# Optimization experiments

Measured on AMD Instinct MI355X. Metric: run time of the kernel, lower is better.

The kernel has to match this reference:

```python
import jax, jax.numpy as jnp
import numpy as np

D_MODEL = 512
D_STATE = 32
EXPAND = 2
D_INNER = D_MODEL * EXPAND
BATCH = 2
SEQ_LEN = 1024


def setup_inputs() -> dict:
    key = jax.random.key(0)
    ks = jax.random.split(key, 8)
    s = lambda fan_in: 1.0 / np.sqrt(fan_in)
    x = jax.random.normal(ks[0], (BATCH, SEQ_LEN, D_MODEL), dtype=jnp.float32)
    Wx = jax.random.uniform(ks[1], (D_INNER, D_MODEL), minval=-s(D_MODEL), maxval=s(D_MODEL))
    Wdt = jax.random.uniform(ks[2], (D_INNER, D_MODEL), minval=-s(D_MODEL), maxval=s(D_MODEL))
    bdt = jax.random.uniform(ks[3], (D_INNER,)) + 1.0  # dt_proj.bias init: rand + 1
    A_log = jnp.log(jax.random.uniform(ks[4], (D_INNER, D_STATE), minval=1e-4, maxval=1.0))
    WB = jax.random.uniform(ks[5], (D_INNER * D_STATE, D_MODEL), minval=-s(D_MODEL), maxval=s(D_MODEL))
    WC = jax.random.uniform(ks[6], (D_INNER * D_STATE, D_MODEL), minval=-s(D_MODEL), maxval=s(D_MODEL))
    Wout = jax.random.uniform(ks[7], (D_MODEL, D_INNER), minval=-s(D_INNER), maxval=s(D_INNER))
    return {"x": x, "Wx": Wx, "Wdt": Wdt, "bdt": bdt, "A_log": A_log,
            "WB": WB, "WC": WC, "Wout": Wout}


def reference(x, Wx, Wdt, bdt, A_log, WB, WC, Wout):
    b, L, _ = x.shape
    d_inner, d_state = A_log.shape

    x_inner = jnp.einsum('bld,ed->ble', x, Wx)                 # (b, L, d_inner)
    delta = jax.nn.softplus(jnp.einsum('bld,ed->ble', x, Wdt) + bdt)
    A = -jnp.exp(A_log.astype(jnp.float32))                    # (d_inner, d_state)
    A_disc = jnp.exp(delta[..., None] * A)                     # (b, L, d_inner, d_state)
    Bm = jnp.einsum('bld,ed->ble', x, WB).reshape(b, L, d_inner, d_state)
    Cm = jnp.einsum('bld,ed->ble', x, WC).reshape(b, L, d_inner, d_state)

    def step(h, inp):
        a_t, b_t, c_t, x_t = inp
        h = a_t * h + b_t * x_t[..., None]                     # (b, d_inner, d_state)
        y = jnp.sum(c_t * h, axis=-1)                          # (b, d_inner)
        return h, y

    h0 = jnp.zeros((b, d_inner, d_state), dtype=x.dtype)
    xs = (jnp.moveaxis(A_disc, 1, 0), jnp.moveaxis(Bm, 1, 0),
          jnp.moveaxis(Cm, 1, 0), jnp.moveaxis(x_inner, 1, 0))
    _, ys = jax.lax.scan(step, h0, xs)                         # ys: (L, b, d_inner)
    y = jnp.moveaxis(ys, 0, 1)
    y = y * jax.nn.sigmoid(y)                                  # SiLU
    return jnp.einsum('ble,de->bld', y, Wout)
```

## Files before the change

### kernel.cpp

```cpp
#include <hip/hip_runtime.h>

#define BATCH   2
#define SEQLEN  1024
#define DMODEL  512
#define DSTATE  32
#define DINNER  1024
#define MROWS   (BATCH*SEQLEN)
#define NPROJ   (2*DINNER + 2*DINNER*DSTATE)

typedef short bf16x8 __attribute__((ext_vector_type(8)));
typedef float f32x4  __attribute__((ext_vector_type(4)));

__device__ __forceinline__ unsigned short f2bf(float f) {
    union { float f; unsigned u; } c; c.f = f;
    unsigned u = c.u;
    u += 0x7fffu + ((u >> 16) & 1u);
    return (unsigned short)(u >> 16);
}
__device__ __forceinline__ float bf2f(unsigned short h) {
    union { unsigned u; float f; } c; c.u = ((unsigned)h) << 16;
    return c.f;
}

__global__ void cast_all(const float4* __restrict__ Wx, const float4* __restrict__ Wdt,
                         const float4* __restrict__ WB, const float4* __restrict__ WC,
                         const float4* __restrict__ x,  const float4* __restrict__ Wout,
                         unsigned short* __restrict__ Wbf,
                         unsigned short* __restrict__ Xbf,
                         unsigned short* __restrict__ Woutbf) {
    const long nWx = 131072, nWdt = 131072, nWB = 4194304, nWC = 4194304;
    const long nWall = nWx + nWdt + nWB + nWC;
    const long nX = 262144, nWo = 131072;
    const long total = nWall + nX + nWo;
    for (long u = (long)blockIdx.x * blockDim.x + threadIdx.x; u < total;
         u += (long)gridDim.x * blockDim.x) {
        float4 v; unsigned short* dst;
        if (u < nWall) {
            if (u < nWx)             v = Wx[u];
            else if (u < nWx+nWdt)   v = Wdt[u - nWx];
            else if (u < nWx+nWdt+nWB) v = WB[u - nWx - nWdt];
            else                     v = WC[u - nWx - nWdt - nWB];
            dst = Wbf + u*4;
        } else if (u < nWall + nX) {
            v = x[u - nWall];       dst = Xbf + (u - nWall)*4;
        } else {
            v = Wout[u - nWall - nX]; dst = Woutbf + (u - nWall - nX)*4;
        }
        ushort4 o; o.x = f2bf(v.x); o.y = f2bf(v.y); o.z = f2bf(v.z); o.w = f2bf(v.w);
        *(ushort4*)dst = o;
    }
}

template<int EPI>
__global__ __launch_bounds__(256)
void gemm_bt(const unsigned short* __restrict__ A, const unsigned short* __restrict__ Bw,
             int K, int N, int t0, int Tchunk, int tgs,
             float* __restrict__ xin, float* __restrict__ dlt,
             unsigned short* __restrict__ Bout, unsigned short* __restrict__ Cout,
             const float* __restrict__ bdt, float* __restrict__ outf) {
    __shared__ unsigned short Asm[2][128*32];
    __shared__ unsigned short Bsm[2][128*32];
    const int tid  = threadIdx.x;
    const int w    = tid >> 6;
    const int lane = tid & 63;
    const int wm   = w >> 1, wn = w & 1;

    const int nx = gridDim.x, ny = gridDim.y;
    int ntile, rtile;
    if ((nx & 7) == 0) {
        const int lin = blockIdx.x + nx * blockIdx.y;
        const int xcd = lin & 7;
        const int sl  = lin >> 3;
        ntile = xcd * (nx >> 3) + sl / ny;
        rtile = sl % ny;
    } else {
        ntile = blockIdx.x; rtile = blockIdx.y;
    }

    const int rr0  = rtile * 128;
    const int bb   = (rr0 >= Tchunk) ? 1 : 0;
    const int grow0 = bb * SEQLEN + t0 + (rr0 - bb * Tchunk);
    const int n0   = ntile * 128;

    f32x4 acc[4][4] = {};

    const unsigned short* Ag = A  + (size_t)grow0 * K;
    const unsigned short* Bg = Bw + (size_t)n0 * K;

    const int c0 = w*64 + lane;
    const int c1 = c0 + 256;
    const int r   = lane & 15;
    const int h16 = lane >> 4;

    const int rowc0 = c0 >> 2, rowc1 = c1 >> 2;
    const int subc0 = (c0 & 3) ^ ((c0 >> 3) & 3);
    const int subc1 = (c1 & 3) ^ ((c1 >> 3) & 3);
    const size_t srcA0 = (size_t)rowc0 * K + subc0 * 8;
    const size_t srcA1 = (size_t)rowc1 * K + subc1 * 8;

    const int nt = K >> 5;

    #define STAGE(k0_, buf_)                                                              \
        do {                                                                              \
            __builtin_amdgcn_global_load_lds(                                             \
                (const __attribute__((address_space(1))) void*)(Ag + srcA0 + (k0_)),      \
                (__attribute__((address_space(3))) void*)(&Asm[(buf_)][w*512]), 16, 0, 0);\
            __builtin_amdgcn_global_load_lds(                                             \
                (const __attribute__((address_space(1))) void*)(Ag + srcA1 + (k0_)),      \
                (__attribute__((address_space(3))) void*)(&Asm[(buf_)][2048 + w*512]), 16, 0, 0); \
            __builtin_amdgcn_global_load_lds(                                             \
                (const __attribute__((address_space(1))) void*)(Bg + srcA0 + (k0_)),      \
                (__attribute__((address_space(3))) void*)(&Bsm[(buf_)][w*512]), 16, 0, 0);\
            __builtin_amdgcn_global_load_lds(                                             \
                (const __attribute__((address_space(1))) void*)(Bg + srcA1 + (k0_)),      \
                (__attribute__((address_space(3))) void*)(&Bsm[(buf_)][2048 + w*512]), 16, 0, 0); \
        } while (0)

    #define COMPUTE(buf_)                                                                 \
        do {                                                                              \
            bf16x8 af[4], bfr[4];                                                         \
            _Pragma("unroll")                                                             \
            for (int i = 0; i < 4; i++) {                                                 \
                const int Ra = wm*64 + i*16 + r;                                          \
                const int Rb = wn*64 + i*16 + r;                                          \
                af[i]  = *(const bf16x8*)(&Asm[(buf_)][Ra*32 + (h16 ^ ((Ra>>1)&3))*8]);   \
                bfr[i] = *(const bf16x8*)(&Bsm[(buf_)][Rb*32 + (h16 ^ ((Rb>>1)&3))*8]);   \
            }                                                                             \
            _Pragma("unroll")                                                             \
            for (int i = 0; i < 4; i++)                                                   \
                _Pragma("unroll")                                                         \
                for (int j = 0; j < 4; j++)                                               \
                    acc[i][j] = __builtin_amdgcn_mfma_f32_16x16x32_bf16(af[i], bfr[j], acc[i][j], 0, 0, 0); \
        } while (0)

    STAGE(0, 0);
    for (int it = 0; it < nt - 1; ++it) {
        const int cur = it & 1;
        STAGE((it + 1) * 32, cur ^ 1);
        asm volatile("s_waitcnt vmcnt(4)" ::: "memory");
        __builtin_amdgcn_s_barrier();
        COMPUTE(cur);
        asm volatile("" ::: "memory");
        __builtin_amdgcn_s_barrier();
        asm volatile("" ::: "memory");
    }
    asm volatile("s_waitcnt vmcnt(0)" ::: "memory");
    __builtin_amdgcn_s_barrier();
    COMPUTE((nt - 1) & 1);

    #undef STAGE
    #undef COMPUTE

    const int q = lane >> 4;
    const int Tg  = 1 << tgs;
    const int NT  = Tg >> 3;
    #pragma unroll
    for (int i = 0; i < 4; i++) {
        const int lr0 = wm*64 + i*16 + q*4;
        #pragma unroll
        for (int j = 0; j < 4; j++) {
            const int ncol = n0 + wn*64 + j*16 + r;
            if (EPI == 0) {
                const int cr   = rr0 + lr0;
                const int lt   = cr - bb*Tchunk;
                const int seg  = lt >> tgs;
                const int tloc = lt & (Tg - 1);
                const int kin  = tloc >> 3;
                const int tin  = tloc & 7;
                const int bs   = bb*8 + seg;
                if (ncol < 1024) {
                    float4 o = {acc[i][j][0], acc[i][j][1], acc[i][j][2], acc[i][j][3]};
                    *(float4*)(xin + ((size_t)bs*1024 + ncol)*Tg + tloc) = o;
                } else if (ncol < 2048) {
                    const float bias = bdt[ncol - 1024];
                    float4 o;
                    {   float z0 = acc[i][j][0] + bias; o.x = (z0 > 20.f) ? z0 : log1pf(__expf(z0));
                        float z1 = acc[i][j][1] + bias; o.y = (z1 > 20.f) ? z1 : log1pf(__expf(z1));
                        float z2 = acc[i][j][2] + bias; o.z = (z2 > 20.f) ? z2 : log1pf(__expf(z2));
                        float z3 = acc[i][j][3] + bias; o.w = (z3 > 20.f) ? z3 : log1pf(__expf(z3)); }
                    *(float4*)(dlt + ((size_t)bs*1024 + (ncol-1024))*Tg + tloc) = o;
                } else if (ncol < 34816) {
                    const int es = ncol - 2048;
                    short4 o;
                    o.x = (short)f2bf(acc[i][j][0]); o.y = (short)f2bf(acc[i][j][1]);
                    o.z = (short)f2bf(acc[i][j][2]); o.w = (short)f2bf(acc[i][j][3]);
                    *(short4*)(Bout + (((size_t)bs*1024 + (es>>5))*NT + kin)*256 + (es&31)*8 + tin) = o;
                } else {
                    const int es = ncol - 34816;
                    short4 o;
                    o.x = (short)f2bf(acc[i][j][0]); o.y = (short)f2bf(acc[i][j][1]);
                    o.z = (short)f2bf(acc[i][j][2]); o.w = (short)f2bf(acc[i][j][3]);
                    *(short4*)(Cout + (((size_t)bs*1024 + (es>>5))*NT + kin)*256 + (es&31)*8 + tin) = o;
                }
            } else {
                #pragma unroll
                for (int t = 0; t < 4; t++)
                    outf[(size_t)(grow0 + lr0 + t)*N + ncol] = acc[i][j][t];
            }
        }
    }
}

__global__ __launch_bounds__(256)
void scan_seg1(const float* __restrict__ dlt, const float* __restrict__ xin,
               const unsigned short* __restrict__ Bbf,
               const float* __restrict__ A_log,
               float* __restrict__ sc_h, float* __restrict__ sc_a,
               int Tg) {
    const int tid = threadIdx.x;
    const int g = tid >> 5, s = tid & 31;
    const int G = blockIdx.x * 8 + g;
    const int seg = blockIdx.y;
    const int b = G >> 10, e = G & 1023;

    const float Aes = -__expf(A_log[e*32 + s]);
    float h = 0.f, ap = 1.f;

    const int NT = Tg >> 3;
    const int bs = b*8 + seg;
    const float* dp = dlt + ((size_t)bs*1024 + e)*Tg;
    const float* xp = xin + ((size_t)bs*1024 + e)*Tg;
    const unsigned short* bp = Bbf + ((size_t)bs*1024 + e)*NT*256 + s*8;

    float4 d0 = *(const float4*)dp, d1 = *(const float4*)(dp+4);
    float4 x0 = *(const float4*)xp, x1 = *(const float4*)(xp+4);
    bf16x8 bv = *(const bf16x8*)bp;

    for (int k = 0; k < NT; ++k) {
        float4 nd0, nd1, nx0, nx1; bf16x8 nbv;
        if (k + 1 < NT) {
            nd0 = *(const float4*)(dp + (k+1)*8); nd1 = *(const float4*)(dp + (k+1)*8 + 4);
            nx0 = *(const float4*)(xp + (k+1)*8); nx1 = *(const float4*)(xp + (k+1)*8 + 4);
            nbv = *(const bf16x8*)(bp + (size_t)(k+1)*256);
        }
        const float db[8] = {d0.x,d0.y,d0.z,d0.w,d1.x,d1.y,d1.z,d1.w};
        const float xb[8] = {x0.x,x0.y,x0.z,x0.w,x1.x,x1.y,x1.z,x1.w};
        #pragma unroll
        for (int j = 0; j < 8; j++) {
            const float a = __expf(db[j] * Aes);
            h = a*h + bf2f((unsigned short)bv[j])*xb[j];
            ap *= a;
        }
        if (k + 1 < NT) { d0=nd0; d1=nd1; x0=nx0; x1=nx1; bv=nbv; }
    }
    sc_h[((size_t)G*8 + seg)*32 + s] = h;
    sc_a[((size_t)G*8 + seg)*32 + s] = ap;
}

__global__ __launch_bounds__(256)
void scan_seg2(const float* __restrict__ sc_h, const float* __restrict__ sc_a,
               float* __restrict__ sc_hin, float* __restrict__ hbuf,
               int first) {
    const int idx = blockIdx.x * 256 + threadIdx.x;
    float h = first ? 0.f : hbuf[idx];
    const int G = idx >> 5, s = idx & 31;
    for (int seg = 0; seg < 8; seg++) {
        const size_t o = ((size_t)G*8 + seg)*32 + s;
        sc_hin[o] = h;
        h = sc_h[o] + sc_a[o]*h;
    }
    hbuf[idx] = h;
}

__global__ __launch_bounds__(256)
void scan_seg3(const float* __restrict__ dlt, const float* __restrict__ xin,
               const unsigned short* __restrict__ Bbf, const unsigned short* __restrict__ Cbf,
               const float* __restrict__ A_log, const float* __restrict__ sc_hin,
               unsigned short* __restrict__ Ybf,
               int t0, int Tg) {
    const int tid = threadIdx.x;
    const int g = tid >> 5, s = tid & 31;
    const int G = blockIdx.x * 8 + g;
    const int seg = blockIdx.y;
    const int b = G >> 10, e = G & 1023;

    const float Aes = -__expf(A_log[e*32 + s]);
    float h = sc_hin[((size_t)G*8 + seg)*32 + s];

    const int NT = Tg >> 3;
    const int bs = b*8 + seg;
    const float* dp = dlt + ((size_t)bs*1024 + e)*Tg;
    const float* xp = xin + ((size_t)bs*1024 + e)*Tg;
    const unsigned short* bp = Bbf + ((size_t)bs*1024 + e)*NT*256 + s*8;
    const unsigned short* cp = Cbf + ((size_t)bs*1024 + e)*NT*256 + s*8;
    const int tbase = t0 + seg*Tg;

    float4 d0 = *(const float4*)dp, d1 = *(const float4*)(dp+4);
    float4 x0 = *(const float4*)xp, x1 = *(const float4*)(xp+4);
    bf16x8 bv = *(const bf16x8*)bp, cv = *(const bf16x8*)cp;

    for (int k = 0; k < NT; ++k) {
        float4 nd0, nd1, nx0, nx1; bf16x8 nbv, ncv;
        if (k + 1 < NT) {
            nd0 = *(const float4*)(dp + (k+1)*8); nd1 = *(const float4*)(dp + (k+1)*8 + 4);
            nx0 = *(const float4*)(xp + (k+1)*8); nx1 = *(const float4*)(xp + (k+1)*8 + 4);
            nbv = *(const bf16x8*)(bp + (size_t)(k+1)*256);
            ncv = *(const bf16x8*)(cp + (size_t)(k+1)*256);
        }
        const float db[8] = {d0.x,d0.y,d0.z,d0.w,d1.x,d1.y,d1.z,d1.w};
        const float xb[8] = {x0.x,x0.y,x0.z,x0.w,x1.x,x1.y,x1.z,x1.w};
        float p[8];
        #pragma unroll
        for (int j = 0; j < 8; j++) {
            const float a = __expf(db[j] * Aes);
            h = a*h + bf2f((unsigned short)bv[j])*xb[j];
            p[j] = bf2f((unsigned short)cv[j])*h;
        }
        #pragma unroll
        for (int i = 0; i < 4; i++) {
            float send = (s & 16) ? p[i] : p[i+4];
            float recv = __shfl_xor(send, 16, 32);
            p[i] = ((s & 16) ? p[i+4] : p[i]) + recv;
        }
        #pragma unroll
        for (int i = 0; i < 2; i++) {
            float send = (s & 8) ? p[i] : p[i+2];
            float recv = __shfl_xor(send, 8, 32);
            p[i] = ((s & 8) ? p[i+2] : p[i]) + recv;
        }
        {
            float send = (s & 4) ? p[0] : p[1];
            float recv = __shfl_xor(send, 4, 32);
            p[0] = ((s & 4) ? p[1] : p[0]) + recv;
        }
        p[0] += __shfl_xor(p[0], 2, 32);
        p[0] += __shfl_xor(p[0], 1, 32);
        if ((s & 3) == 0) {
            const int tl = s >> 2;
            const float qv = p[0];
            const float y = qv * __builtin_amdgcn_rcpf(1.f + __expf(-qv));
            Ybf[(size_t)b*1048576 + e + (size_t)(tbase + k*8 + tl)*1024] = f2bf(y);
        }
        if (k + 1 < NT) { d0=nd0; d1=nd1; x0=nx0; x1=nx1; bv=nbv; cv=ncv; }
    }
}

extern "C" void kernel_launch(void* const* d_in, const int* in_sizes, int n_in,
                              void* d_out, int out_size, void* d_ws, size_t ws_size,
                              hipStream_t stream) {
    const float* x     = (const float*)d_in[0];
    const float* Wx    = (const float*)d_in[1];
    const float* Wdt   = (const float*)d_in[2];
    const float* bdt   = (const float*)d_in[3];
    const float* A_log = (const float*)d_in[4];
    const float* WB    = (const float*)d_in[5];
    const float* WC    = (const float*)d_in[6];
    const float* Wout  = (const float*)d_in[7];

    char* ws = (char*)d_ws;
    unsigned short* Wbf    = (unsigned short*)(ws);
    unsigned short* Xbf    = (unsigned short*)(ws + 69206016);
    unsigned short* Woutbf = (unsigned short*)(ws + 71303168);
    float*          xin    = (float*)        (ws + 72351744);
    float*          dlt    = (float*)        (ws + 80740352);
    unsigned short* Ybf    = (unsigned short*)(ws + 89128960);
    float*          hbuf   = (float*)        (ws + 93323264);
    float*          sc_h   = (float*)        (ws + 93585408);
    float*          sc_a   = (float*)        (ws + 95682560);
    float*          sc_hin = (float*)        (ws + 97779712);
    unsigned short* Bbf    = (unsigned short*)(ws + 99876864);
    const size_t fixedB = 99876864;

    int T = 128;
    const int cands[4] = {1024, 512, 256, 128};
    for (int ci = 0; ci < 4; ci++) {
        if (fixedB + (size_t)2 * cands[ci] * 131072 <= ws_size) { T = cands[ci]; break; }
    }
    unsigned short* Cbf = Bbf + (size_t)T * 65536;

    const int Tg = T / 8;
    int tgs = 0; while ((1 << tgs) < Tg) tgs++;

    cast_all<<<dim3(2048), dim3(256), 0, stream>>>(
        (const float4*)Wx, (const float4*)Wdt, (const float4*)WB, (const float4*)WC,
        (const float4*)x, (const float4*)Wout, Wbf, Xbf, Woutbf);

    const int NC = SEQLEN / T;
    for (int c = 0; c < NC; c++) {
        const int t0 = c * T;
        gemm_bt<0><<<dim3(NPROJ/128, 2*T/128), dim3(256), 0, stream>>>(
            Xbf, Wbf, DMODEL, NPROJ, t0, T, tgs, xin, dlt, Bbf, Cbf, bdt, nullptr);
        scan_seg1<<<dim3(256, 8), dim3(256), 0, stream>>>(
            dlt, xin, Bbf, A_log, sc_h, sc_a, Tg);
        scan_seg2<<<dim3(256), dim3(256), 0, stream>>>(
            sc_h, sc_a, sc_hin, hbuf, (c == 0) ? 1 : 0);
        scan_seg3<<<dim3(256, 8), dim3(256), 0, stream>>>(
            dlt, xin, Bbf, Cbf, A_log, sc_hin, Ybf, t0, Tg);
    }

    gemm_bt<1><<<dim3(DMODEL/128, MROWS/128), dim3(256), 0, stream>>>(
        Ybf, Woutbf, DINNER, DMODEL, 0, MROWS, 0, nullptr, nullptr, nullptr, nullptr, nullptr,
        (float*)d_out);
}
```

Measured before the change: 413.8 us.

## Fuse three-pass chunked scan into one kernel with shared-memory segment carry

Replaces the three scan kernels (per-segment local scan, serial carry propagation, rescan with output) with one kernel. Each block handles one (batch, channel) row, and its 8 warps cover the 8 time segments. Segment summaries are combined through shared memory, and each warp keeps its B values in registers between the two passes so B is read from global memory once. This removes two launches per chunk and the sc_h/sc_a/sc_hin global round trips. In exchange it adds register pressure (up to 16 bf16x8 vectors per thread) and drops the explicit software prefetch of the next step's data.

```diff
diff --git a/kernel.cpp b/kernel.cpp
--- a/kernel.cpp
+++ b/kernel.cpp
@@ -201,122 +201,84 @@
     }
 }
 
+template<int NT>
 __global__ __launch_bounds__(256)
-void scan_seg1(const float* __restrict__ dlt, const float* __restrict__ xin,
-               const unsigned short* __restrict__ Bbf,
-               const float* __restrict__ A_log,
-               float* __restrict__ sc_h, float* __restrict__ sc_a,
-               int Tg) {
+void scan_fused(const float* __restrict__ dlt, const float* __restrict__ xin,
+                const unsigned short* __restrict__ Bbf, const unsigned short* __restrict__ Cbf,
+                const float* __restrict__ A_log,
+                unsigned short* __restrict__ Ybf, float* __restrict__ hbuf,
+                int t0, int first) {
     const int tid = threadIdx.x;
     const int g = tid >> 5, s = tid & 31;
-    const int G = blockIdx.x * 8 + g;
-    const int seg = blockIdx.y;
+    const int G = blockIdx.x;
     const int b = G >> 10, e = G & 1023;
+    const int bs = b*8 + g;
+    const int Tg = NT * 8;
 
     const float Aes = -__expf(A_log[e*32 + s]);
-    float h = 0.f, ap = 1.f;
-
-    const int NT = Tg >> 3;
-    const int bs = b*8 + seg;
-    const float* dp = dlt + ((size_t)bs*1024 + e)*Tg;
-    const float* xp = xin + ((size_t)bs*1024 + e)*Tg;
-    const unsigned short* bp = Bbf + ((size_t)bs*1024 + e)*NT*256 + s*8;
-
-    float4 d0 = *(const float4*)dp, d1 = *(const float4*)(dp+4);
-    float4 x0 = *(const float4*)xp, x1 = *(const float4*)(xp+4);
-    bf16x8 bv = *(const bf16x8*)bp;
-
-    for (int k = 0; k < NT; ++k) {
-        float4 nd0, nd1, nx0, nx1; bf16x8 nbv;
-        if (k + 1 < NT) {
-            nd0 = *(const float4*)(dp + (k+1)*8); nd1 = *(const float4*)(dp + (k+1)*8 + 4);
-            nx0 = *(const float4*)(xp + (k+1)*8); nx1 = *(const float4*)(xp + (k+1)*8 + 4);
-            nbv = *(const bf16x8*)(bp + (size_t)(k+1)*256);
-        }
-        const float db[8] = {d0.x,d0.y,d0.z,d0.w,d1.x,d1.y,d1.z,d1.w};
-        const float xb[8] = {x0.x,x0.y,x0.z,x0.w,x1.x,x1.y,x1.z,x1.w};
-        #pragma unroll
-        for (int j = 0; j < 8; j++) {
-            const float a = __expf(db[j] * Aes);
-            h = a*h + bf2f((unsigned short)bv[j])*xb[j];
-            ap *= a;
-        }
-        if (k + 1 < NT) { d0=nd0; d1=nd1; x0=nx0; x1=nx1; bv=nbv; }
-    }
-    sc_h[((size_t)G*8 + seg)*32 + s] = h;
-    sc_a[((size_t)G*8 + seg)*32 + s] = ap;
-}
-
-__global__ __launch_bounds__(256)
-void scan_seg2(const float* __restrict__ sc_h, const float* __restrict__ sc_a,
-               float* __restrict__ sc_hin, float* __restrict__ hbuf,
-               int first) {
-    const int idx = blockIdx.x * 256 + threadIdx.x;
-    float h = first ? 0.f : hbuf[idx];
-    const int G = idx >> 5, s = idx & 31;
-    for (int seg = 0; seg < 8; seg++) {
-        const size_t o = ((size_t)G*8 + seg)*32 + s;
-        sc_hin[o] = h;
-        h = sc_h[o] + sc_a[o]*h;
-    }
-    hbuf[idx] = h;
-}
-
-__global__ __launch_bounds__(256)
-void scan_seg3(const float* __restrict__ dlt, const float* __restrict__ xin,
-               const unsigned short* __restrict__ Bbf, const unsigned short* __restrict__ Cbf,
-               const float* __restrict__ A_log, const float* __restrict__ sc_hin,
-               unsigned short* __restrict__ Ybf,
-               int t0, int Tg) {
-    const int tid = threadIdx.x;
-    const int g = tid >> 5, s = tid & 31;
-    const int G = blockIdx.x * 8 + g;
-    const int seg = blockIdx.y;
-    const int b = G >> 10, e = G & 1023;
-
-    const float Aes = -__expf(A_log[e*32 + s]);
-    float h = sc_hin[((size_t)G*8 + seg)*32 + s];
-
-    const int NT = Tg >> 3;
-    const int bs = b*8 + seg;
+
     const float* dp = dlt + ((size_t)bs*1024 + e)*Tg;
     const float* xp = xin + ((size_t)bs*1024 + e)*Tg;
     const unsigned short* bp = Bbf + ((size_t)bs*1024 + e)*NT*256 + s*8;
     const unsigned short* cp = Cbf + ((size_t)bs*1024 + e)*NT*256 + s*8;
-    const int tbase = t0 + seg*Tg;
-
-    float4 d0 = *(const float4*)dp, d1 = *(const float4*)(dp+4);
-    float4 x0 = *(const float4*)xp, x1 = *(const float4*)(xp+4);
-    bf16x8 bv = *(const bf16x8*)bp, cv = *(const bf16x8*)cp;
-
-    for (int k = 0; k < NT; ++k) {
-        float4 nd0, nd1, nx0, nx1; bf16x8 nbv, ncv;
-        if (k + 1 < NT) {
-            nd0 = *(const float4*)(dp + (k+1)*8); nd1 = *(const float4*)(dp + (k+1)*8 + 4);
-            nx0 = *(const float4*)(xp + (k+1)*8); nx1 = *(const float4*)(xp + (k+1)*8 + 4);
-            nbv = *(const bf16x8*)(bp + (size_t)(k+1)*256);
-            ncv = *(const bf16x8*)(cp + (size_t)(k+1)*256);
-        }
+
+    bf16x8 Bc[NT];
+    #pragma unroll
+    for (int k = 0; k < NT; k++) Bc[k] = *(const bf16x8*)(bp + (size_t)k*256);
+
+    float h = 0.f, ap = 1.f;
+    #pragma unroll
+    for (int k = 0; k < NT; k++) {
+        const float4 d0 = *(const float4*)(dp + k*8), d1 = *(const float4*)(dp + k*8 + 4);
+        const float4 x0 = *(const float4*)(xp + k*8), x1 = *(const float4*)(xp + k*8 + 4);
+        const float db[8] = {d0.x,d0.y,d0.z,d0.w,d1.x,d1.y,d1.z,d1.w};
+        const float xb[8] = {x0.x,x0.y,x0.z,x0.w,x1.x,x1.y,x1.z,x1.w};
+        #pragma unroll
+        for (int j = 0; j < 8; j++) {
+            const float a = __expf(db[j] * Aes);
+            h = a*h + bf2f((unsigned short)Bc[k][j])*xb[j];
+            ap *= a;
+        }
+    }
+
+    __shared__ float Lh[8][32];
+    __shared__ float La[8][32];
+    Lh[g][s] = h; La[g][s] = ap;
+    __syncthreads();
+    float hin = first ? 0.f : hbuf[(size_t)G*32 + s];
+    #pragma unroll
+    for (int j = 0; j < 7; j++) {
+        if (j < g) hin = La[j][s]*hin + Lh[j][s];
+    }
+    if (g == 7) hbuf[(size_t)G*32 + s] = La[7][s]*hin + Lh[7][s];
+
+    h = hin;
+    const int tbase = t0 + g*Tg;
+    #pragma unroll
+    for (int k = 0; k < NT; k++) {
+        const bf16x8 cv = *(const bf16x8*)(cp + (size_t)k*256);
+        const float4 d0 = *(const float4*)(dp + k*8), d1 = *(const float4*)(dp + k*8 + 4);
+        const float4 x0 = *(const float4*)(xp + k*8), x1 = *(const float4*)(xp + k*8 + 4);
         const float db[8] = {d0.x,d0.y,d0.z,d0.w,d1.x,d1.y,d1.z,d1.w};
         const float xb[8] = {x0.x,x0.y,x0.z,x0.w,x1.x,x1.y,x1.z,x1.w};
         float p[8];
         #pragma unroll
         for (int j = 0; j < 8; j++) {
             const float a = __expf(db[j] * Aes);
-            h = a*h + bf2f((unsigned short)bv[j])*xb[j];
+            h = a*h + bf2f((unsigned short)Bc[k][j])*xb[j];
             p[j] = bf2f((unsigned short)cv[j])*h;
         }
         #pragma unroll
-        for (int i = 0; i < 4; i++) {
-            float send = (s & 16) ? p[i] : p[i+4];
+        for (int i2 = 0; i2 < 4; i2++) {
+            float send = (s & 16) ? p[i2] : p[i2+4];
             float recv = __shfl_xor(send, 16, 32);
-            p[i] = ((s & 16) ? p[i+4] : p[i]) + recv;
-        }
-        #pragma unroll
-        for (int i = 0; i < 2; i++) {
-            float send = (s & 8) ? p[i] : p[i+2];
+            p[i2] = ((s & 16) ? p[i2+4] : p[i2]) + recv;
+        }
+        #pragma unroll
+        for (int i2 = 0; i2 < 2; i2++) {
+            float send = (s & 8) ? p[i2] : p[i2+2];
             float recv = __shfl_xor(send, 8, 32);
-            p[i] = ((s & 8) ? p[i+2] : p[i]) + recv;
+            p[i2] = ((s & 8) ? p[i2+2] : p[i2]) + recv;
         }
         {
             float send = (s & 4) ? p[0] : p[1];
@@ -331,7 +293,6 @@
             const float y = qv * __builtin_amdgcn_rcpf(1.f + __expf(-qv));
             Ybf[(size_t)b*1048576 + e + (size_t)(tbase + k*8 + tl)*1024] = f2bf(y);
         }
-        if (k + 1 < NT) { d0=nd0; d1=nd1; x0=nx0; x1=nx1; bv=nbv; cv=ncv; }
     }
 }
 
@@ -355,9 +316,6 @@
     float*          dlt    = (float*)        (ws + 80740352);
     unsigned short* Ybf    = (unsigned short*)(ws + 89128960);
     float*          hbuf   = (float*)        (ws + 93323264);
-    float*          sc_h   = (float*)        (ws + 93585408);
-    float*          sc_a   = (float*)        (ws + 95682560);
-    float*          sc_hin = (float*)        (ws + 97779712);
     unsigned short* Bbf    = (unsigned short*)(ws + 99876864);
     const size_t fixedB = 99876864;
 
@@ -370,6 +328,7 @@
 
     const int Tg = T / 8;
     int tgs = 0; while ((1 << tgs) < Tg) tgs++;
+    const int NT = Tg / 8;
 
     cast_all<<<dim3(2048), dim3(256), 0, stream>>>(
         (const float4*)Wx, (const float4*)Wdt, (const float4*)WB, (const float4*)WC,
@@ -378,14 +337,21 @@
     const int NC = SEQLEN / T;
     for (int c = 0; c < NC; c++) {
         const int t0 = c * T;
+        const int first = (c == 0) ? 1 : 0;
         gemm_bt<0><<<dim3(NPROJ/128, 2*T/128), dim3(256), 0, stream>>>(
             Xbf, Wbf, DMODEL, NPROJ, t0, T, tgs, xin, dlt, Bbf, Cbf, bdt, nullptr);
-        scan_seg1<<<dim3(256, 8), dim3(256), 0, stream>>>(
-            dlt, xin, Bbf, A_log, sc_h, sc_a, Tg);
-        scan_seg2<<<dim3(256), dim3(256), 0, stream>>>(
-            sc_h, sc_a, sc_hin, hbuf, (c == 0) ? 1 : 0);
-        scan_seg3<<<dim3(256, 8), dim3(256), 0, stream>>>(
-            dlt, xin, Bbf, Cbf, A_log, sc_hin, Ybf, t0, Tg);
+        if (NT == 16)
+            scan_fused<16><<<dim3(2048), dim3(256), 0, stream>>>(
+                dlt, xin, Bbf, Cbf, A_log, Ybf, hbuf, t0, first);
+        else if (NT == 8)
+            scan_fused<8><<<dim3(2048), dim3(256), 0, stream>>>(
+                dlt, xin, Bbf, Cbf, A_log, Ybf, hbuf, t0, first);
+        else if (NT == 4)
+            scan_fused<4><<<dim3(2048), dim3(256), 0, stream>>>(
+                dlt, xin, Bbf, Cbf, A_log, Ybf, hbuf, t0, first);
+        else
+            scan_fused<2><<<dim3(2048), dim3(256), 0, stream>>>(
+                dlt, xin, Bbf, Cbf, A_log, Ybf, hbuf, t0, first);
     }
 
     gemm_bt<1><<<dim3(DMODEL/128, MROWS/128), dim3(256), 0, stream>>>(
```

Result: faster. 398.4 us (-3.7%).
